# Kernel optimization log

Hardware: AMD Instinct MI355X
Metric: run time of the kernel (lower is better)

## Reference

```python
import jax, jax.numpy as jnp
import numpy as np

B, N = 64, 1500
F_MIN, F_MAX = 0.5, 3.0  # HR band in Hz (30-180 bpm)
SAMPLING_F = 0.002       # frequency grid step -> F = 1251 frequencies
FS = 30.0                # video frame rate


def setup_inputs() -> dict:
    key = jax.random.key(0)
    k1, k2 = jax.random.split(key)
    x = jax.random.normal(k1, (B, N), dtype=jnp.float32)
    # true frequencies inside the searched band
    f_true = jax.random.uniform(k2, (B,), dtype=jnp.float32, minval=F_MIN, maxval=F_MAX)
    fs = jnp.full((B,), FS, dtype=jnp.float32)
    deltas = jnp.zeros((B,), dtype=jnp.float32)  # accepted but unused by the loss
    return {
        "x": x,
        "f_true": f_true,
        "fs": fs,
        "deltas": deltas,
        "sampling_f": SAMPLING_F,
        "f_range": (F_MIN, F_MAX),
    }


def reference(x, f_true, fs, deltas, sampling_f, f_range):
    f_min, f_max = f_range
    # frequency grid, same semantics as torch.arange(f_min, f_max+step, step)
    f_values = jnp.arange(f_min, f_max + sampling_f, sampling_f, dtype=jnp.float32)  # [F]
    n = jnp.arange(x.shape[1], dtype=jnp.float32)  # [N] time indices
    # angles[b,f,n] = 2*pi * f_values[f] * n / fs[b]  (fs varies per sample)
    phase = (2.0 * jnp.pi) * (f_values[None, :, None] * n[None, None, :]) / fs[:, None, None]  # [B,F,N]
    # PSD at each grid frequency: (sum x cos)^2 + (sum x sin)^2, batched as one contraction
    cos_terms = jnp.einsum('bn,bfn->bf', x, jnp.cos(phase))  # [B,F]
    sin_terms = jnp.einsum('bn,bfn->bf', x, jnp.sin(phase))  # [B,F]
    psd = cos_terms ** 2 + sin_terms ** 2                    # [B,F]
    log_lik = jnp.log(jax.nn.softmax(psd, axis=1) + 1e-8)    # [B,F]
    # index of grid frequency closest to f_true (non-differentiable gather index)
    idx = jnp.argmin(jnp.abs(f_values[None, :] - f_true[:, None]), axis=1)  # [B]
    per_sample = -jnp.take_along_axis(log_lik, idx[:, None], axis=1)[:, 0]  # [B]
    return jnp.mean(per_sample)
```

## Files before the change

kernel.cpp:

```cpp
#include <hip/hip_runtime.h>

#define BATCH 64
#define NSAMP 1500
#define NFREQ 1251
#define NSEG  5
#define SEGLEN 300
#define FBLK  256
#define FCHUNKS 5

__global__ __launch_bounds__(256) void goertzel_kernel(
    const float* __restrict__ x,
    const float* __restrict__ fs,
    const float* __restrict__ sampling_f,
    const float* __restrict__ f_range,
    float2* __restrict__ pcs,
    float* __restrict__ out)
{
    __shared__ float4 xs4[SEGLEN / 4];
    const int b   = blockIdx.x;
    const int seg = blockIdx.z;
    const int tid = threadIdx.x;
    const int n0  = seg * SEGLEN;

    if (b == 0 && seg == 0 && blockIdx.y == 0 && tid == 0) out[0] = 0.0f;

    const float4* xg = reinterpret_cast<const float4*>(x + b * NSAMP + n0);
    for (int i = tid; i < SEGLEN / 4; i += FBLK) xs4[i] = xg[i];
    __syncthreads();

    const int fidx = blockIdx.y * FBLK + tid;
    if (fidx >= NFREQ) return;

    const float f_min = f_range[0];
    const float step  = sampling_f[0];
    const float delta = (f_min + step) - f_min;
    const float fv    = f_min + (float)fidx * delta;

    const float rho = fv / fs[b];
    float rf = rho - floorf(rho);
    const float coef = 2.0f * __builtin_amdgcn_cosf(rf);

    float s1 = 0.0f, s2 = 0.0f;
#pragma unroll 5
    for (int k = 0; k < SEGLEN / 4; ++k) {
        float4 v = xs4[k];
        float t;
        t = fmaf(coef, s1, v.x - s2); s2 = s1; s1 = t;
        t = fmaf(coef, s1, v.y - s2); s2 = s1; s1 = t;
        t = fmaf(coef, s1, v.z - s2); s2 = s1; s1 = t;
        t = fmaf(coef, s1, v.w - s2); s2 = s1; s1 = t;
    }

    float aM  = (float)SEGLEN * rho;        aM  -= floorf(aM);
    float aM1 = (float)(SEGLEN - 1) * rho;  aM1 -= floorf(aM1);
    float a0  = (float)n0 * rho;            a0  -= floorf(a0);
    const float cM  = __builtin_amdgcn_cosf(aM);
    const float sM  = __builtin_amdgcn_sinf(aM);
    const float cM1 = __builtin_amdgcn_cosf(aM1);
    const float sM1 = __builtin_amdgcn_sinf(aM1);
    const float c0  = __builtin_amdgcn_cosf(a0);
    const float s0  = __builtin_amdgcn_sinf(a0);

    const float Cl = cM1 * s1 - cM * s2;
    const float Sl = sM1 * s1 - sM * s2;
    const float C  = c0 * Cl - s0 * Sl;
    const float S  = s0 * Cl + c0 * Sl;

    pcs[(b * NSEG + seg) * NFREQ + fidx] = make_float2(C, S);
}

__global__ __launch_bounds__(256) void loss_kernel(
    const float2* __restrict__ pcs,
    const float* __restrict__ f_true,
    const float* __restrict__ sampling_f,
    const float* __restrict__ f_range,
    float* __restrict__ out)
{
    const int b    = blockIdx.x;
    const int tid  = threadIdx.x;
    const int wave = tid >> 6;
    const int lane = tid & 63;

    __shared__ float wm[4];
    __shared__ float wl[4];
    __shared__ float s_pidx;

    const float f_min = f_range[0];
    const float step  = sampling_f[0];
    const float delta = (f_min + step) - f_min;
    const float ft    = f_true[b];

    int iq = (int)((ft - f_min) / delta + 0.5f);
    int lo = iq - 2; if (lo < 0) lo = 0;
    int hi = iq + 2; if (hi > NFREQ - 1) hi = NFREQ - 1;
    int   idx   = lo;
    float bestd = fabsf((f_min + (float)lo * delta) - ft);
    for (int i = lo + 1; i <= hi; ++i) {
        float d = fabsf((f_min + (float)i * delta) - ft);
        if (d < bestd) { bestd = d; idx = i; }
    }

    float m = -INFINITY, l = 0.0f;
    for (int i = tid; i < NFREQ; i += 256) {
        float c = 0.0f, s = 0.0f;
#pragma unroll
        for (int g = 0; g < NSEG; ++g) {
            float2 v = pcs[(b * NSEG + g) * NFREQ + i];
            c += v.x; s += v.y;
        }
        float v = fmaf(c, c, s * s);
        if (i == idx) s_pidx = v;
        float mn = fmaxf(m, v);
        l = l * __expf(m - mn) + __expf(v - mn);
        m = mn;
    }
    for (int off = 32; off > 0; off >>= 1) {
        float m2 = __shfl_down(m, off);
        float l2 = __shfl_down(l, off);
        float mn = fmaxf(m, m2);
        l = l * __expf(m - mn) + l2 * __expf(m2 - mn);
        m = mn;
    }
    if (lane == 0) { wm[wave] = m; wl[wave] = l; }
    __syncthreads();

    if (tid == 0) {
        float gm = wm[0], gl = wl[0];
#pragma unroll
        for (int w = 1; w < 4; ++w) {
            float mn = fmaxf(gm, wm[w]);
            gl = gl * __expf(gm - mn) + wl[w] * __expf(wm[w] - mn);
            gm = mn;
        }
        float sm  = __expf(s_pidx - gm) / gl;
        float per = -logf(sm + 1e-8f);
        atomicAdd(out, per * (1.0f / (float)BATCH));
    }
}

extern "C" void kernel_launch(void* const* d_in, const int* in_sizes, int n_in,
                              void* d_out, int out_size, void* d_ws, size_t ws_size,
                              hipStream_t stream) {
    const float* x          = (const float*)d_in[0];
    const float* f_true     = (const float*)d_in[1];
    const float* fs         = (const float*)d_in[2];
    const float* sampling_f = (const float*)d_in[4];
    const float* f_range    = (const float*)d_in[5];

    float2* pcs = (float2*)d_ws;

    dim3 g1(BATCH, FCHUNKS, NSEG);
    goertzel_kernel<<<g1, FBLK, 0, stream>>>(x, fs, sampling_f, f_range, pcs,
                                             (float*)d_out);
    loss_kernel<<<BATCH, 256, 0, stream>>>(pcs, f_true, sampling_f, f_range,
                                           (float*)d_out);
}
```

Before: 74.50 us.

## Compute all five Goertzel segments per thread and emit PSD directly

Each thread now runs five independent Goertzel recurrences, one per time segment, and interleaves them in the same loop instead of spreading the segments across separate blocks. The segment results are combined into the PSD inside the thread, so the kernel writes one float per frequency instead of five partial complex sums. The goal is more instruction-level parallelism from independent dependency chains and less workspace traffic for the loss kernel. In exchange the grid shrinks fivefold (320 blocks) and each thread needs more registers, which may reduce occupancy.

```diff
diff --git a/kernel.cpp b/kernel.cpp
--- a/kernel.cpp
+++ b/kernel.cpp
@@ -8,24 +8,22 @@
 #define FBLK  256
 #define FCHUNKS 5
 
-__global__ __launch_bounds__(256) void goertzel_kernel(
+__global__ __launch_bounds__(256) void goertzel_psd_kernel(
     const float* __restrict__ x,
     const float* __restrict__ fs,
     const float* __restrict__ sampling_f,
     const float* __restrict__ f_range,
-    float2* __restrict__ pcs,
+    float* __restrict__ psd,
     float* __restrict__ out)
 {
-    __shared__ float4 xs4[SEGLEN / 4];
+    __shared__ float4 xs4[NSAMP / 4];
     const int b   = blockIdx.x;
-    const int seg = blockIdx.z;
     const int tid = threadIdx.x;
-    const int n0  = seg * SEGLEN;
 
-    if (b == 0 && seg == 0 && blockIdx.y == 0 && tid == 0) out[0] = 0.0f;
+    if (b == 0 && blockIdx.y == 0 && tid == 0) out[0] = 0.0f;
 
-    const float4* xg = reinterpret_cast<const float4*>(x + b * NSAMP + n0);
-    for (int i = tid; i < SEGLEN / 4; i += FBLK) xs4[i] = xg[i];
+    const float4* xg = reinterpret_cast<const float4*>(x + b * NSAMP);
+    for (int i = tid; i < NSAMP / 4; i += FBLK) xs4[i] = xg[i];
     __syncthreads();
 
     const int fidx = blockIdx.y * FBLK + tid;
@@ -40,37 +38,47 @@
     float rf = rho - floorf(rho);
     const float coef = 2.0f * __builtin_amdgcn_cosf(rf);
 
-    float s1 = 0.0f, s2 = 0.0f;
-#pragma unroll 5
+    float s1[NSEG], s2[NSEG];
+#pragma unroll
+    for (int g = 0; g < NSEG; ++g) { s1[g] = 0.0f; s2[g] = 0.0f; }
+
+#pragma unroll 3
     for (int k = 0; k < SEGLEN / 4; ++k) {
-        float4 v = xs4[k];
-        float t;
-        t = fmaf(coef, s1, v.x - s2); s2 = s1; s1 = t;
-        t = fmaf(coef, s1, v.y - s2); s2 = s1; s1 = t;
-        t = fmaf(coef, s1, v.z - s2); s2 = s1; s1 = t;
-        t = fmaf(coef, s1, v.w - s2); s2 = s1; s1 = t;
+#pragma unroll
+        for (int g = 0; g < NSEG; ++g) {
+            float4 v = xs4[g * (SEGLEN / 4) + k];
+            float t;
+            t = fmaf(coef, s1[g], v.x - s2[g]); s2[g] = s1[g]; s1[g] = t;
+            t = fmaf(coef, s1[g], v.y - s2[g]); s2[g] = s1[g]; s1[g] = t;
+            t = fmaf(coef, s1[g], v.z - s2[g]); s2[g] = s1[g]; s1[g] = t;
+            t = fmaf(coef, s1[g], v.w - s2[g]); s2[g] = s1[g]; s1[g] = t;
+        }
     }
 
     float aM  = (float)SEGLEN * rho;        aM  -= floorf(aM);
     float aM1 = (float)(SEGLEN - 1) * rho;  aM1 -= floorf(aM1);
-    float a0  = (float)n0 * rho;            a0  -= floorf(a0);
     const float cM  = __builtin_amdgcn_cosf(aM);
     const float sM  = __builtin_amdgcn_sinf(aM);
     const float cM1 = __builtin_amdgcn_cosf(aM1);
     const float sM1 = __builtin_amdgcn_sinf(aM1);
-    const float c0  = __builtin_amdgcn_cosf(a0);
-    const float s0  = __builtin_amdgcn_sinf(a0);
 
-    const float Cl = cM1 * s1 - cM * s2;
-    const float Sl = sM1 * s1 - sM * s2;
-    const float C  = c0 * Cl - s0 * Sl;
-    const float S  = s0 * Cl + c0 * Sl;
+    float C = 0.0f, S = 0.0f;
+#pragma unroll
+    for (int g = 0; g < NSEG; ++g) {
+        float a0 = (float)(g * SEGLEN) * rho;  a0 -= floorf(a0);
+        const float c0 = __builtin_amdgcn_cosf(a0);
+        const float s0 = __builtin_amdgcn_sinf(a0);
+        const float Cl = cM1 * s1[g] - cM * s2[g];
+        const float Sl = sM1 * s1[g] - sM * s2[g];
+        C += c0 * Cl - s0 * Sl;
+        S += s0 * Cl + c0 * Sl;
+    }
 
-    pcs[(b * NSEG + seg) * NFREQ + fidx] = make_float2(C, S);
+    psd[b * NFREQ + fidx] = fmaf(C, C, S * S);
 }
 
 __global__ __launch_bounds__(256) void loss_kernel(
-    const float2* __restrict__ pcs,
+    const float* __restrict__ psd,
     const float* __restrict__ f_true,
     const float* __restrict__ sampling_f,
     const float* __restrict__ f_range,
@@ -102,13 +110,7 @@
 
     float m = -INFINITY, l = 0.0f;
     for (int i = tid; i < NFREQ; i += 256) {
-        float c = 0.0f, s = 0.0f;
-#pragma unroll
-        for (int g = 0; g < NSEG; ++g) {
-            float2 v = pcs[(b * NSEG + g) * NFREQ + i];
-            c += v.x; s += v.y;
-        }
-        float v = fmaf(c, c, s * s);
+        float v = psd[b * NFREQ + i];
         if (i == idx) s_pidx = v;
         float mn = fmaxf(m, v);
         l = l * __expf(m - mn) + __expf(v - mn);
@@ -147,11 +149,11 @@
     const float* sampling_f = (const float*)d_in[4];
     const float* f_range    = (const float*)d_in[5];
 
-    float2* pcs = (float2*)d_ws;
+    float* psd = (float*)d_ws;
 
-    dim3 g1(BATCH, FCHUNKS, NSEG);
-    goertzel_kernel<<<g1, FBLK, 0, stream>>>(x, fs, sampling_f, f_range, pcs,
-                                             (float*)d_out);
-    loss_kernel<<<BATCH, 256, 0, stream>>>(pcs, f_true, sampling_f, f_range,
+    dim3 g1(BATCH, FCHUNKS);
+    goertzel_psd_kernel<<<g1, FBLK, 0, stream>>>(x, fs, sampling_f, f_range,
+                                                 psd, (float*)d_out);
+    loss_kernel<<<BATCH, 256, 0, stream>>>(psd, f_true, sampling_f, f_range,
                                            (float*)d_out);
 }
```

Result: slower. 79.78 us (+7.1%).
